# Optimization experiments

Hardware: AMD Instinct MI355X
Metric: run time of the kernel (lower is better)

## Reference

```python
import jax, jax.numpy as jnp
import numpy as np

N = 8192
IN_DIM = 256
OUT_DIM = 256


def setup_inputs() -> dict:
    key = jax.random.key(0)
    k1, k2, k3, k4 = jax.random.split(key, 4)
    x = jax.random.normal(k1, (N, IN_DIM), dtype=jnp.float32)
    adj = jax.random.uniform(k2, (N, N), dtype=jnp.float32)
    # nn.Linear(in_dim, out_dim): weight [out,in], bias [out]. Store W as [in,out].
    bound = 1.0 / np.sqrt(IN_DIM)
    W = jax.random.uniform(k3, (IN_DIM, OUT_DIM), dtype=jnp.float32, minval=-bound, maxval=bound)
    b = jax.random.uniform(k4, (OUT_DIM,), dtype=jnp.float32, minval=-bound, maxval=bound)
    return {"x": x, "adj": adj, "W": W, "b": b}


def reference(x, adj, W, b):
    # ReLU( D^{-1/2} (A + I) D^{-1/2} X W + b )
    # A_hat = adj + I; degree = A_hat.sum(axis=1)
    n = adj.shape[0]
    A_hat = adj + jnp.eye(n, dtype=adj.dtype)
    degree = A_hat.sum(axis=1)
    d_inv_sqrt = degree ** -0.5  # [N]
    # D^{-1/2} @ A_hat @ D^{-1/2} == row-scale then col-scale (no NxN diag matmuls)
    A_norm = A_hat * d_inv_sqrt[:, None] * d_inv_sqrt[None, :]
    out = A_norm @ x          # [N, in_dim]
    out = out @ W + b         # [N, out_dim]
    return jax.nn.relu(out)
```

## Files before the change

### kernel.cpp

```cpp
#include <hip/hip_runtime.h>
#include <hip/hip_bf16.h>


typedef __attribute__((ext_vector_type(8))) short short8;
typedef __attribute__((ext_vector_type(4))) short short4v;
typedef __attribute__((ext_vector_type(4))) float floatx4;

#define GLDS16(g, l) __builtin_amdgcn_global_load_lds(\
    (const __attribute__((address_space(1))) void*)(g), \
    (__attribute__((address_space(3))) void*)(l), 16, 0, 0)

__device__ __forceinline__ unsigned short f2b(float f) {
  unsigned int x = __builtin_bit_cast(unsigned int, f);
  unsigned int r = (x + 0x7fffu + ((x >> 16) & 1u)) >> 16;
  return (unsigned short)r;
}

__global__ __launch_bounds__(256) void k_prep(
    const float* __restrict__ adj, const float* __restrict__ W,
    const float* __restrict__ X, float* __restrict__ s,
    unsigned short* __restrict__ WT, unsigned short* __restrict__ Xb) {
  __shared__ float part[4];
  const int b = blockIdx.x, t = threadIdx.x;
  if (b < 8192) {
    const float4* row = (const float4*)(adj + (size_t)b * 8192);
    float sum = 0.f;
#pragma unroll
    for (int q = 0; q < 8; ++q) {
      float4 v = row[t + q * 256];
      sum += v.x + v.y + v.z + v.w;
    }
#pragma unroll
    for (int o = 32; o > 0; o >>= 1) sum += __shfl_down(sum, o, 64);
    if ((t & 63) == 0) part[t >> 6] = sum;
    __syncthreads();
    if (t == 0) s[b] = rsqrtf(part[0] + part[1] + part[2] + part[3] + 1.0f);
  } else if (b < 8256) {
    const int wb = b - 8192;
#pragma unroll
    for (int q = 0; q < 4; ++q) {
      int i = wb * 1024 + q * 256 + t;
      WT[i] = f2b(W[(i & 255) * 256 + (i >> 8)]);
    }
  } else {
    const int xb = b - 8256;
#pragma unroll
    for (int q = 0; q < 8; ++q) {
      int i = xb * 2048 + q * 256 + t;
      Xb[i] = f2b(X[i]);
    }
  }
}

__global__ __launch_bounds__(256) void k_xw(
    const unsigned short* __restrict__ Xb, const unsigned short* __restrict__ WT,
    const float* __restrict__ bias, const float* __restrict__ s,
    float* __restrict__ Zd, unsigned short* __restrict__ Zsb) {
  __shared__ __align__(16) unsigned short ldsX[64 * 256];
  __shared__ __align__(16) unsigned short ldsW[64 * 256];
  __shared__ __align__(16) unsigned short ldsT[64 * 72];
  const int t = threadIdx.x, l = t & 63, w = t >> 6;
  const int quad = l >> 4, nl = l & 15;
  const int m0 = blockIdx.x * 64, n0 = blockIdx.y * 64;
#pragma unroll
  for (int r = 0; r < 8; ++r) {
    int sl = r * 256 + t;
    int kc = sl >> 6, mm = sl & 63;
    GLDS16(Xb + (m0 + mm) * 256 + kc * 8, (char*)ldsX + sl * 16);
    GLDS16(WT + (n0 + mm) * 256 + kc * 8, (char*)ldsW + sl * 16);
  }
  __syncthreads();
  const int wm = w & 1, wn = w >> 1;
  floatx4 acc[2][2] = {};
#pragma unroll
  for (int kk = 0; kk < 8; ++kk) {
    int kc = kk * 4 + quad;
    short8 af[2], bf[2];
#pragma unroll
    for (int i = 0; i < 2; ++i) {
      af[i] = *(const short8*)&ldsX[(kc * 64 + wm * 32 + i * 16 + nl) * 8];
      bf[i] = *(const short8*)&ldsW[(kc * 64 + wn * 32 + i * 16 + nl) * 8];
    }
#pragma unroll
    for (int mi = 0; mi < 2; ++mi)
#pragma unroll
      for (int ni = 0; ni < 2; ++ni)
        acc[mi][ni] = __builtin_amdgcn_mfma_f32_16x16x32_bf16(af[mi], bf[ni], acc[mi][ni], 0, 0, 0);
  }
#pragma unroll
  for (int mi = 0; mi < 2; ++mi)
#pragma unroll
    for (int ni = 0; ni < 2; ++ni)
#pragma unroll
      for (int r = 0; r < 4; ++r) {
        int row = m0 + wm * 32 + mi * 16 + quad * 4 + r;
        int col = n0 + wn * 32 + ni * 16 + nl;
        float v = acc[mi][ni][r];
        float sr = s[row];
        Zd[row * 256 + col] = sr * sr * v + bias[col];
        ldsT[(col - n0) * 72 + (row - m0)] = f2b(sr * v);
      }
  __syncthreads();
#pragma unroll
  for (int h = 0; h < 2; ++h) {
    int c = h * 256 + t;
    int kc = c >> 6, nn = c & 63;
    short8 val = *(const short8*)&ldsT[nn * 72 + kc * 8];
    *(short8*)(Zsb + (size_t)blockIdx.x * 16384 + kc * 2048 + (n0 + nn) * 8) = val;
  }
}

__global__ __launch_bounds__(512) void k_main(
    const float* __restrict__ adj, const unsigned short* __restrict__ Zsb,
    const float* __restrict__ s, const float* __restrict__ Zd,
    float* __restrict__ out) {
  __shared__ __align__(16) char ldsA[2][8 * 544];
  __shared__ __align__(16) unsigned short ldsB[2][64 * 256];
  const int t = threadIdx.x, l = t & 63, w = t >> 6;
  const int quad = l >> 4, nl = l & 15;
  const int m0 = blockIdx.x * 32;
  const int aM = t >> 4, aC = t & 15;
  const float* aSrc = adj + (size_t)(m0 + aM) * 8192 + aC * 4;
  const int aOff = (aC >> 1) * 544 + aM * 16 + (aC & 1) * 8;
  floatx4 acc[2][2] = {};

  float4 av = *(const float4*)(aSrc);
#pragma unroll
  for (int r = 0; r < 4; ++r) {
    int sl = r * 512 + t;
    GLDS16(Zsb + (size_t)sl * 8, (char*)ldsB[0] + sl * 16);
  }
  {
    short4v ab = {(short)f2b(av.x), (short)f2b(av.y), (short)f2b(av.z), (short)f2b(av.w)};
    *(short4v*)(ldsA[0] + aOff) = ab;
  }
  __syncthreads();

  for (int kt = 0; kt < 128; ++kt) {
    const int cur = kt & 1, nxt = cur ^ 1;
    const int ktn = (kt < 127) ? kt + 1 : 127;
    av = *(const float4*)(aSrc + (size_t)ktn * 64);
#pragma unroll
    for (int r = 0; r < 4; ++r) {
      int sl = r * 512 + t;
      GLDS16(Zsb + (size_t)(ktn * 2048 + sl) * 8, (char*)ldsB[nxt] + sl * 16);
    }
#pragma unroll
    for (int kk = 0; kk < 2; ++kk) {
      int kc = kk * 4 + quad;
      short8 af[2], bf[2];
      af[0] = *(const short8*)(ldsA[cur] + kc * 544 + nl * 16);
      af[1] = *(const short8*)(ldsA[cur] + kc * 544 + (16 + nl) * 16);
      bf[0] = *(const short8*)&ldsB[cur][(kc * 256 + w * 32 + nl) * 8];
      bf[1] = *(const short8*)&ldsB[cur][(kc * 256 + w * 32 + 16 + nl) * 8];
      acc[0][0] = __builtin_amdgcn_mfma_f32_16x16x32_bf16(af[0], bf[0], acc[0][0], 0, 0, 0);
      acc[0][1] = __builtin_amdgcn_mfma_f32_16x16x32_bf16(af[0], bf[1], acc[0][1], 0, 0, 0);
      acc[1][0] = __builtin_amdgcn_mfma_f32_16x16x32_bf16(af[1], bf[0], acc[1][0], 0, 0, 0);
      acc[1][1] = __builtin_amdgcn_mfma_f32_16x16x32_bf16(af[1], bf[1], acc[1][1], 0, 0, 0);
    }
    {
      short4v ab = {(short)f2b(av.x), (short)f2b(av.y), (short)f2b(av.z), (short)f2b(av.w)};
      *(short4v*)(ldsA[nxt] + aOff) = ab;
    }
    __syncthreads();
  }

#pragma unroll
  for (int mi = 0; mi < 2; ++mi)
#pragma unroll
    for (int ni = 0; ni < 2; ++ni)
#pragma unroll
      for (int r = 0; r < 4; ++r) {
        int row = m0 + mi * 16 + quad * 4 + r;
        int col = w * 32 + ni * 16 + nl;
        float v = s[row] * acc[mi][ni][r] + Zd[row * 256 + col];
        out[row * 256 + col] = v > 0.f ? v : 0.f;
      }
}

extern "C" void kernel_launch(void* const* d_in, const int* in_sizes, int n_in,
                              void* d_out, int out_size, void* d_ws, size_t ws_size,
                              hipStream_t stream) {
  const float* X    = (const float*)d_in[0];
  const float* adj  = (const float*)d_in[1];
  const float* W    = (const float*)d_in[2];
  const float* bias = (const float*)d_in[3];
  float* out = (float*)d_out;

  char* ws = (char*)d_ws;
  float* s            = (float*)(ws);
  unsigned short* WT  = (unsigned short*)(ws + 32768);
  unsigned short* Xb  = (unsigned short*)(ws + 262144);
  float* Zd           = (float*)(ws + (8 << 20));
  unsigned short* Zsb = (unsigned short*)(ws + (16 << 20));

  hipLaunchKernelGGL(k_prep, dim3(9280), dim3(256), 0, stream, adj, W, X, s, WT, Xb);
  hipLaunchKernelGGL(k_xw, dim3(128, 4), dim3(256), 0, stream, Xb, WT, bias, s, Zd, Zsb);
  hipLaunchKernelGGL(k_main, dim3(256), dim3(512), 0, stream, adj, Zsb, s, Zd, out);
}
```

Baseline: 528.6 us.

## Pre-convert adjacency to tiled bf16 during degree pass and restructure main GEMM

The prep kernel now reads adj once, computes the row degrees and writes a bf16 copy of adj already in MFMA tile layout. The main kernel can then stream half the bytes directly into LDS with global_load_lds, using a triple-buffered A and double-buffered B pipeline gated by vmcnt waits. The X·W product moves to a simple fp32 FMA kernel, and the main kernel uses 512 blocks of 128 threads, each wave owning a 32x64 output tile. The cost is an extra 128MB bf16 write and re-read plus a workspace-size check, with the old path kept as a fallback.

```diff
diff --git a/kernel.cpp b/kernel.cpp
--- a/kernel.cpp
+++ b/kernel.cpp
@@ -16,7 +16,181 @@
   return (unsigned short)r;
 }
 
+
 __global__ __launch_bounds__(256) void k_prep(
+    const float* __restrict__ adj, float* __restrict__ s,
+    unsigned short* __restrict__ adjb) {
+  __shared__ __align__(16) unsigned short tile[256 * 8];
+  __shared__ float part[512];
+  const int t = threadIdx.x;
+  const int bm = blockIdx.x, m0 = bm * 32;
+  const int mA = t >> 4, mB = 16 + (t >> 4);
+  const int c_ = t & 15;
+  const float* src0 = adj + (size_t)(m0 + mA) * 8192 + c_ * 4;
+  const float* src1 = adj + (size_t)(m0 + mB) * 8192 + c_ * 4;
+  const int kc = c_ >> 1, h = c_ & 1;
+  unsigned short* dst0 = tile + (size_t)(kc * 32 + ((mA + 4 * kc) & 31)) * 8 + h * 4;
+  unsigned short* dst1 = tile + (size_t)(kc * 32 + ((mB + 4 * kc) & 31)) * 8 + h * 4;
+  const int kcg = t >> 5, mmg = t & 31;
+  const unsigned short* osrc = tile + (size_t)(kcg * 32 + ((mmg + 4 * kcg) & 31)) * 8;
+  unsigned short* obase = adjb + (size_t)bm * 128 * 2048 + t * 8;
+  float rs0 = 0.f, rs1 = 0.f;
+  float4 c0 = *(const float4*)(src0);
+  float4 c1 = *(const float4*)(src1);
+  for (int kt = 0; kt < 128; ++kt) {
+    const int ktn = (kt + 1) & 127;
+    float4 n0v = *(const float4*)(src0 + ktn * 64);
+    float4 n1v = *(const float4*)(src1 + ktn * 64);
+    rs0 += c0.x + c0.y + c0.z + c0.w;
+    rs1 += c1.x + c1.y + c1.z + c1.w;
+    short4v b0 = {(short)f2b(c0.x), (short)f2b(c0.y), (short)f2b(c0.z), (short)f2b(c0.w)};
+    short4v b1 = {(short)f2b(c1.x), (short)f2b(c1.y), (short)f2b(c1.z), (short)f2b(c1.w)};
+    *(short4v*)dst0 = b0;
+    *(short4v*)dst1 = b1;
+    __syncthreads();
+    short8 v = *(const short8*)osrc;
+    *(short8*)(obase + (size_t)kt * 2048) = v;
+    __syncthreads();
+    c0 = n0v; c1 = n1v;
+  }
+  part[t] = rs0; part[256 + t] = rs1;
+  __syncthreads();
+  if (t < 32) {
+    float sum = 1.0f;
+#pragma unroll
+    for (int j = 0; j < 16; ++j) sum += part[t * 16 + j];
+    s[m0 + t] = rsqrtf(sum);
+  }
+}
+
+__global__ __launch_bounds__(256) void k_xw(
+    const float* __restrict__ X, const float* __restrict__ W,
+    const float* __restrict__ bias, const float* __restrict__ s,
+    float* __restrict__ Zd, unsigned short* __restrict__ Zsb) {
+  __shared__ unsigned short ldsT[256 * 36];
+  const int t = threadIdx.x, l = t & 63, w = t >> 6;
+  const int m0 = blockIdx.x * 32;
+  const int r0 = w * 8;
+  const int n0 = l * 4;
+  const float* Xp = X + (size_t)(m0 + r0) * 256;
+  float acc[8][4] = {};
+#pragma unroll 2
+  for (int k = 0; k < 256; k += 4) {
+    float4 wv[4];
+#pragma unroll
+    for (int j = 0; j < 4; ++j) wv[j] = *(const float4*)(W + (size_t)(k + j) * 256 + n0);
+#pragma unroll
+    for (int r = 0; r < 8; ++r) {
+      float4 xv = *(const float4*)(Xp + r * 256 + k);
+      const float xs[4] = {xv.x, xv.y, xv.z, xv.w};
+#pragma unroll
+      for (int j = 0; j < 4; ++j) {
+        acc[r][0] += xs[j] * wv[j].x;
+        acc[r][1] += xs[j] * wv[j].y;
+        acc[r][2] += xs[j] * wv[j].z;
+        acc[r][3] += xs[j] * wv[j].w;
+      }
+    }
+  }
+  const float4 bv = *(const float4*)(bias + n0);
+  const int kt = m0 >> 6, hh = (m0 >> 5) & 1;
+#pragma unroll
+  for (int r = 0; r < 8; ++r) {
+    const int row = m0 + r0 + r;
+    const float sr = s[row];
+    float4 zd;
+    zd.x = sr * sr * acc[r][0] + bv.x;
+    zd.y = sr * sr * acc[r][1] + bv.y;
+    zd.z = sr * sr * acc[r][2] + bv.z;
+    zd.w = sr * sr * acc[r][3] + bv.w;
+    *(float4*)(Zd + (size_t)row * 256 + n0) = zd;
+#pragma unroll
+    for (int n = 0; n < 4; ++n)
+      ldsT[(size_t)(n0 + n) * 36 + (r0 + r)] = f2b(sr * acc[r][n]);
+  }
+  __syncthreads();
+#pragma unroll
+  for (int c = 0; c < 4; ++c) {
+    const unsigned short* p = ldsT + (size_t)t * 36 + c * 8;
+    short4v lo = *(const short4v*)(p);
+    short4v hi = *(const short4v*)(p + 4);
+    short8 vv;
+    vv[0] = lo[0]; vv[1] = lo[1]; vv[2] = lo[2]; vv[3] = lo[3];
+    vv[4] = hi[0]; vv[5] = hi[1]; vv[6] = hi[2]; vv[7] = hi[3];
+    *(short8*)(Zsb + ((size_t)kt * 2048 + (hh * 4 + c) * 256 + t) * 8) = vv;
+  }
+}
+
+__global__ __launch_bounds__(128) void k_main(
+    const unsigned short* __restrict__ adjb, const unsigned short* __restrict__ Zsb,
+    const float* __restrict__ s, const float* __restrict__ Zd,
+    float* __restrict__ out) {
+  __shared__ __align__(16) char lds[57344];
+  const int t = threadIdx.x, l = t & 63, w = t >> 6;
+  const int quad = l >> 4, nl = l & 15;
+  const int bm = blockIdx.x >> 1;
+  const int m0 = bm * 32;
+  const int n0 = (blockIdx.x & 1) * 128 + w * 64;
+  char* bufA = lds + w * 12288;
+  char* bufB = lds + 24576 + w * 16384;
+  const unsigned short* aB = adjb + (size_t)bm * 128 * 2048;
+  floatx4 acc[2][4] = {};
+
+#pragma unroll
+  for (int r = 0; r < 4; ++r)
+    GLDS16(aB + (size_t)(r * 64 + l) * 8, bufA + (r * 64 + l) * 16);
+#pragma unroll
+  for (int r = 0; r < 8; ++r)
+    GLDS16(Zsb + (size_t)(r * 256 + n0 + l) * 8, bufB + (r * 64 + l) * 16);
+#pragma unroll
+  for (int r = 0; r < 4; ++r)
+    GLDS16(aB + (size_t)(256 + r * 64 + l) * 8, bufA + 4096 + (r * 64 + l) * 16);
+
+  for (int kt = 0; kt < 128; ++kt) {
+    const int ktb = kt < 127 ? kt + 1 : 127;
+    const int kta = kt < 126 ? kt + 2 : 127;
+    char* dstB = bufB + (ktb & 1) * 8192;
+    char* dstA = bufA + (kta % 3) * 4096;
+#pragma unroll
+    for (int r = 0; r < 8; ++r)
+      GLDS16(Zsb + (size_t)(ktb * 2048 + r * 256 + n0 + l) * 8, dstB + (r * 64 + l) * 16);
+#pragma unroll
+    for (int r = 0; r < 4; ++r)
+      GLDS16(aB + (size_t)(kta * 256 + r * 64 + l) * 8, dstA + (r * 64 + l) * 16);
+    asm volatile("s_waitcnt vmcnt(16)" ::: "memory");
+    const char* rA = bufA + (kt % 3) * 4096;
+    const char* rB = bufB + (kt & 1) * 8192;
+#pragma unroll
+    for (int kk = 0; kk < 2; ++kk) {
+      const int kc = kk * 4 + quad;
+      short8 af[2], bf[4];
+      af[0] = *(const short8*)(rA + (kc * 32 + nl) * 16);
+      af[1] = *(const short8*)(rA + (kc * 32 + 16 + nl) * 16);
+#pragma unroll
+      for (int nf = 0; nf < 4; ++nf)
+        bf[nf] = *(const short8*)(rB + (kc * 64 + nf * 16 + nl) * 16);
+#pragma unroll
+      for (int mi = 0; mi < 2; ++mi)
+#pragma unroll
+        for (int nf = 0; nf < 4; ++nf)
+          acc[mi][nf] = __builtin_amdgcn_mfma_f32_16x16x32_bf16(af[mi], bf[nf], acc[mi][nf], 0, 0, 0);
+    }
+  }
+
+#pragma unroll
+  for (int mi = 0; mi < 2; ++mi)
+#pragma unroll
+    for (int nf = 0; nf < 4; ++nf)
+#pragma unroll
+      for (int r = 0; r < 4; ++r) {
+        const int row = m0 + mi * 16 + quad * 4 + r;
+        const int col = n0 + nf * 16 + nl;
+        float v = s[row] * acc[mi][nf][r] + Zd[row * 256 + col];
+        out[row * 256 + col] = v > 0.f ? v : 0.f;
+      }
+}
+
+__global__ __launch_bounds__(256) void fb_prep(
     const float* __restrict__ adj, const float* __restrict__ W,
     const float* __restrict__ X, float* __restrict__ s,
     unsigned short* __restrict__ WT, unsigned short* __restrict__ Xb) {
@@ -52,7 +226,7 @@
   }
 }
 
-__global__ __launch_bounds__(256) void k_xw(
+__global__ __launch_bounds__(256) void fb_xw(
     const unsigned short* __restrict__ Xb, const unsigned short* __restrict__ WT,
     const float* __restrict__ bias, const float* __restrict__ s,
     float* __restrict__ Zd, unsigned short* __restrict__ Zsb) {
@@ -102,15 +276,15 @@
       }
   __syncthreads();
 #pragma unroll
-  for (int h = 0; h < 2; ++h) {
-    int c = h * 256 + t;
+  for (int hq = 0; hq < 2; ++hq) {
+    int c = hq * 256 + t;
     int kc = c >> 6, nn = c & 63;
     short8 val = *(const short8*)&ldsT[nn * 72 + kc * 8];
     *(short8*)(Zsb + (size_t)blockIdx.x * 16384 + kc * 2048 + (n0 + nn) * 8) = val;
   }
 }
 
-__global__ __launch_bounds__(512) void k_main(
+__global__ __launch_bounds__(512) void fb_main(
     const float* __restrict__ adj, const unsigned short* __restrict__ Zsb,
     const float* __restrict__ s, const float* __restrict__ Zd,
     float* __restrict__ out) {
@@ -123,7 +297,6 @@
   const float* aSrc = adj + (size_t)(m0 + aM) * 8192 + aC * 4;
   const int aOff = (aC >> 1) * 544 + aM * 16 + (aC & 1) * 8;
   floatx4 acc[2][2] = {};
-
   float4 av = *(const float4*)(aSrc);
 #pragma unroll
   for (int r = 0; r < 4; ++r) {
@@ -135,7 +308,6 @@
     *(short4v*)(ldsA[0] + aOff) = ab;
   }
   __syncthreads();
-
   for (int kt = 0; kt < 128; ++kt) {
     const int cur = kt & 1, nxt = cur ^ 1;
     const int ktn = (kt < 127) ? kt + 1 : 127;
@@ -164,7 +336,6 @@
     }
     __syncthreads();
   }
-
 #pragma unroll
   for (int mi = 0; mi < 2; ++mi)
 #pragma unroll
@@ -186,15 +357,25 @@
   const float* W    = (const float*)d_in[2];
   const float* bias = (const float*)d_in[3];
   float* out = (float*)d_out;
-
   char* ws = (char*)d_ws;
-  float* s            = (float*)(ws);
-  unsigned short* WT  = (unsigned short*)(ws + 32768);
-  unsigned short* Xb  = (unsigned short*)(ws + 262144);
-  float* Zd           = (float*)(ws + (8 << 20));
-  unsigned short* Zsb = (unsigned short*)(ws + (16 << 20));
-
-  hipLaunchKernelGGL(k_prep, dim3(9280), dim3(256), 0, stream, adj, W, X, s, WT, Xb);
-  hipLaunchKernelGGL(k_xw, dim3(128, 4), dim3(256), 0, stream, Xb, WT, bias, s, Zd, Zsb);
-  hipLaunchKernelGGL(k_main, dim3(256), dim3(512), 0, stream, adj, Zsb, s, Zd, out);
-}
+
+  const size_t need = (size_t)142 * 1024 * 1024;
+  if (ws_size >= need) {
+    float* s             = (float*)(ws);
+    unsigned short* Zsb  = (unsigned short*)(ws + (1 << 20));
+    float* Zd            = (float*)(ws + (5 << 20));
+    unsigned short* adjb = (unsigned short*)(ws + ((size_t)13 << 20));
+    hipLaunchKernelGGL(k_prep, dim3(256), dim3(256), 0, stream, adj, s, adjb);
+    hipLaunchKernelGGL(k_xw, dim3(256), dim3(256), 0, stream, X, W, bias, s, Zd, Zsb);
+    hipLaunchKernelGGL(k_main, dim3(512), dim3(128), 0, stream, adjb, Zsb, s, Zd, out);
+  } else {
+    float* s            = (float*)(ws);
+    unsigned short* WT  = (unsigned short*)(ws + 32768);
+    unsigned short* Xb  = (unsigned short*)(ws + 262144);
+    float* Zd           = (float*)(ws + (8 << 20));
+    unsigned short* Zsb = (unsigned short*)(ws + (16 << 20));
+    hipLaunchKernelGGL(fb_prep, dim3(9280), dim3(256), 0, stream, adj, W, X, s, WT, Xb);
+    hipLaunchKernelGGL(fb_xw, dim3(128, 4), dim3(256), 0, stream, Xb, WT, bias, s, Zd, Zsb);
+    hipLaunchKernelGGL(fb_main, dim3(256), dim3(512), 0, stream, adj, Zsb, s, Zd, out);
+  }
+}
```

Result: slower. 546.2 us (+3.3%).
